# Kernel optimization log

Hardware: AMD Instinct MI355X
Metric: run time of the kernel (lower is better)

The kernel has to match this reference:

```python
import jax, jax.numpy as jnp
import numpy as np

N, D_IN, D_OUT, E = 100000, 64, 64, 800000
C_IN, C_OUT = 1.0, 1.0
MAX_NORM = 1e6   # manifold.max_norm clamp used by PseudoHypAgg
EPS = 1e-15
BALL_EPS = 4e-3  # Poincare-ball projection margin (fp32)


def _artanh(x):
    return jnp.arctanh(jnp.clip(x, -1 + 1e-7, 1 - 1e-7))


def _proj(x, c):
    # project onto the open Poincare ball of curvature c
    sqrt_c = jnp.sqrt(c)
    norm = jnp.clip(jnp.linalg.norm(x, axis=-1, keepdims=True), EPS)
    maxn = (1.0 - BALL_EPS) / sqrt_c
    return jnp.where(norm > maxn, x / norm * maxn, x)


def _expmap0(u, c):
    sqrt_c = jnp.sqrt(c)
    n = jnp.clip(jnp.linalg.norm(u, axis=-1, keepdims=True), EPS)
    return jnp.tanh(sqrt_c * n) * u / (sqrt_c * n)


def _logmap0(p, c):
    sqrt_c = jnp.sqrt(c)
    n = jnp.clip(jnp.linalg.norm(p, axis=-1, keepdims=True), EPS)
    return _artanh(sqrt_c * n) * p / (sqrt_c * n)


def _mobius_add(x, y, c):
    x2 = jnp.sum(x * x, -1, keepdims=True)
    y2 = jnp.sum(y * y, -1, keepdims=True)
    xy = jnp.sum(x * y, -1, keepdims=True)
    num = (1 + 2 * c * xy + c * y2) * x + (1 - c * x2) * y
    den = 1 + 2 * c * xy + c * c * x2 * y2
    return num / jnp.clip(den, EPS)


def _mobius_matvec(M, x, c):
    sqrt_c = jnp.sqrt(c)
    x_norm = jnp.clip(jnp.linalg.norm(x, axis=-1, keepdims=True), EPS)
    mx = x @ M.T  # [N, D_OUT]
    mx_norm = jnp.clip(jnp.linalg.norm(mx, axis=-1, keepdims=True), EPS)
    res = jnp.tanh(mx_norm / x_norm * _artanh(sqrt_c * x_norm)) * mx / (mx_norm * sqrt_c)
    zero = jnp.all(mx == 0, axis=-1, keepdims=True)
    return jnp.where(zero, jnp.zeros_like(res), res)


def setup_inputs() -> dict:
    key = jax.random.key(0)
    k1, k2, k3, k4, k5, k6 = jax.random.split(key, 6)
    # node features: small-norm points inside the unit ball
    x = _proj(0.05 * jax.random.normal(k1, (N, D_IN), jnp.float32), C_IN)
    W = jax.random.normal(k2, (D_OUT, D_IN), jnp.float32) / np.float32(np.sqrt(D_IN))
    b = 0.01 * jax.random.normal(k3, (D_OUT,), jnp.float32)
    edge_row = jax.random.randint(k4, (E,), 0, N, jnp.int32)
    edge_col = jax.random.randint(k5, (E,), 0, N, jnp.int32)
    edge_val = jax.random.uniform(k6, (E,), jnp.float32) / 16.0  # ~normalized adj weights
    return {"x": x, "W": W, "b": b, "edge_row": edge_row,
            "edge_col": edge_col, "edge_val": edge_val}


def reference(x, W, b, edge_row, edge_col, edge_val):
    # --- PseudoHypLinear (eval mode: dropout inactive) ---
    mv = _mobius_matvec(W, x, C_IN)
    res = _proj(mv, C_IN)
    hyp_b = _proj(_expmap0(b[None, :], C_IN), C_IN)  # proj_tan0 is identity on the ball
    h = _proj(_mobius_add(res, hyp_b, C_IN), C_IN)
    # --- PseudoHypAgg (use_att=False): spmm in tangent space at origin ---
    x_t = _logmap0(h, C_IN)                              # [N, D_OUT]
    msg = edge_val[:, None] * x_t[edge_col]              # [E, D_OUT]
    support_t = jax.ops.segment_sum(msg, edge_row, num_segments=N)
    support_t = jnp.minimum(support_t, MAX_NORM)         # clamp(max=manifold.max_norm)
    h = _proj(_expmap0(support_t, C_IN), C_IN)           # proj_tan0 identity
    # --- PseudoHypAct: act in tangent at origin (c_in), re-embed with c_out ---
    xt = jax.nn.relu(_logmap0(h, C_IN))
    return _proj(_expmap0(xt, C_OUT), C_OUT)
```

## Files before the change

kernel.cpp:

```cpp
#include <hip/hip_runtime.h>
#include <hip/hip_fp16.h>
#include <math.h>

#define DD 64
#define BK 128
#define BCAP 2048
#define NBKT_MAX 800
#define CHUNK 8192
constexpr float FEPS = 1e-15f;
constexpr float MAXN = 1.0f - 4e-3f;

__device__ __forceinline__ float wsum(float v) {
    v += __shfl_xor(v, 32);
    v += __shfl_xor(v, 16);
    v += __shfl_xor(v, 8);
    v += __shfl_xor(v, 4);
    v += __shfl_xor(v, 2);
    v += __shfl_xor(v, 1);
    return v;
}

__device__ __forceinline__ int wave_incl_scan(int v) {
    int lane = threadIdx.x & 63;
    #pragma unroll
    for (int d = 1; d < 64; d <<= 1) {
        int t = __shfl_up(v, d);
        if (lane >= d) v += t;
    }
    return v;
}

__device__ __forceinline__ float artanh_c(float x) {
    x = fminf(fmaxf(x, -1.f + 1e-7f), 1.f - 1e-7f);
    return 0.5f * logf((1.f + x) / (1.f - x));
}

__global__ void khb_kernel(const float* __restrict__ b, float* __restrict__ hbuf) {
    int lane = threadIdx.x;
    float bv = b[lane];
    float n2 = wsum(bv * bv);
    float n = fmaxf(sqrtf(n2), FEPS);
    float th = tanhf(n);
    float p = th * (bv / n);
    float pn = th * (sqrtf(n2) / n);
    float pn_c = fmaxf(pn, FEPS);
    if (pn_c > MAXN) p *= MAXN / pn_c;
    float p2 = wsum(p * p);
    hbuf[lane] = p;
    if (lane == 0) hbuf[DD] = p2;
}

__global__ __launch_bounds__(512) void klinear(
    const float* __restrict__ x, const float* __restrict__ W,
    const float* __restrict__ hbuf, __half* __restrict__ xth, int n_nodes) {
    __shared__ float tile[DD * 65];
    __shared__ float red0[8][DD];
    __shared__ float red1[8][DD];
    const int t = threadIdx.x;
    const int lane = t & 63;
    const int w = t >> 6;
    const int n0 = blockIdx.x * DD;

    #pragma unroll
    for (int rep = 0; rep < 2; ++rep) {
        int i = rep * 512 + t;
        int nd = i >> 4, q = i & 15;
        int node = n0 + nd;
        const float4* src = reinterpret_cast<const float4*>(
            x + (size_t)(node < n_nodes ? node : 0) * DD);
        float4 v = src[q];
        float* d = &tile[nd * 65 + q * 4];
        d[0] = v.x; d[1] = v.y; d[2] = v.z; d[3] = v.w;
    }
    __syncthreads();

    const int jbase = __builtin_amdgcn_readfirstlane(w) * 8;
    float mx[8] = {0.f, 0.f, 0.f, 0.f, 0.f, 0.f, 0.f, 0.f};
    float xn2 = 0.f;
    #pragma unroll
    for (int kk = 0; kk < 4; ++kk) {
        float xv[16];
        #pragma unroll
        for (int ki = 0; ki < 16; ++ki)
            xv[ki] = tile[lane * 65 + kk * 16 + ki];
        #pragma unroll
        for (int ki = 0; ki < 16; ++ki)
            xn2 = fmaf(xv[ki], xv[ki], xn2);
        #pragma unroll
        for (int jj = 0; jj < 8; ++jj) {
            const float* Wr = W + (jbase + jj) * DD + kk * 16;
            float a = mx[jj];
            #pragma unroll
            for (int ki = 0; ki < 16; ++ki) a = fmaf(Wr[ki], xv[ki], a);
            mx[jj] = a;
        }
    }
    float mx2p = 0.f, mxhp = 0.f;
    #pragma unroll
    for (int jj = 0; jj < 8; ++jj) {
        mx2p = fmaf(mx[jj], mx[jj], mx2p);
        mxhp = fmaf(mx[jj], hbuf[jbase + jj], mxhp);
    }
    red0[w][lane] = mx2p;
    red1[w][lane] = mxhp;
    __syncthreads();
    float mx2 = 0.f, mxh = 0.f;
    #pragma unroll
    for (int ww = 0; ww < 8; ++ww) {
        mx2 += red0[ww][lane];
        mxh += red1[ww][lane];
    }

    float xn = fmaxf(sqrtf(xn2), FEPS);
    float mxn = fmaxf(sqrtf(mx2), FEPS);
    float th = tanhf((mxn / xn) * artanh_c(xn));
    float sres = (mx2 == 0.f) ? 0.f : th / mxn;
    float rn = (mx2 == 0.f) ? 0.f : th * (sqrtf(mx2) / mxn);
    float rn_c = fmaxf(rn, FEPS);
    float s1 = (rn_c > MAXN) ? sres * (MAXN / rn_c) : sres;
    float x2r = s1 * s1 * mx2;
    float xy = s1 * mxh;
    float y2 = hbuf[DD];
    float ca = 1.f + 2.f * xy + y2;
    float cb = 1.f - x2r;
    float rden = 1.f / fmaxf(1.f + 2.f * xy + x2r * y2, FEPS);
    float al = ca * s1 * rden;
    float be = cb * rden;
    float h2 = al * al * mx2 + 2.f * al * be * mxh + be * be * y2;
    float hn = fmaxf(sqrtf(h2), FEPS);
    float sh = 1.f;
    if (hn > MAXN) { sh = MAXN / hn; hn = MAXN; }
    float su = sh * (artanh_c(hn) / hn);
    float A = su * al, B = su * be;

    #pragma unroll
    for (int jj = 0; jj < 8; ++jj)
        tile[lane * 65 + jbase + jj] = fmaf(A, mx[jj], B * hbuf[jbase + jj]);
    __syncthreads();

    uint2* dst = reinterpret_cast<uint2*>(xth + (size_t)n0 * DD);
    #pragma unroll
    for (int rep = 0; rep < 2; ++rep) {
        int i = rep * 512 + t;
        int nd = i >> 4, q = i & 15;
        if (n0 + nd < n_nodes) {
            const float* s = &tile[nd * 65 + q * 4];
            __half2 h0 = __floats2half2_rn(s[0], s[1]);
            __half2 h1 = __floats2half2_rn(s[2], s[3]);
            uint2 o;
            o.x = *reinterpret_cast<unsigned int*>(&h0);
            o.y = *reinterpret_cast<unsigned int*>(&h1);
            dst[i] = o;
        }
    }
}

__global__ __launch_bounds__(512) void kbin(
    const int* __restrict__ erow, const int* __restrict__ ecol,
    const float* __restrict__ eval_, int* __restrict__ gcnt,
    int2* __restrict__ binned, int nbkt, int n_edges) {
    __shared__ int lcnt[NBKT_MAX];
    __shared__ int goff[NBKT_MAX];
    const int t = threadIdx.x;
    const int eb = blockIdx.x * CHUNK;
    for (int i = t; i < nbkt; i += 512) lcnt[i] = 0;
    __syncthreads();
    int rk[16];
    int rowv[16];
    #pragma unroll
    for (int i = 0; i < 16; ++i) {
        int e = eb + i * 512 + t;
        rk[i] = -1;
        if (e < n_edges) {
            int r = erow[e];
            rowv[i] = r;
            int bkt = r >> 7;
            int rank = atomicAdd(&lcnt[bkt], 1);
            rk[i] = (bkt << 13) | rank;
        }
    }
    __syncthreads();
    for (int i = t; i < nbkt; i += 512) {
        int c = lcnt[i];
        if (c > 0) goff[i] = atomicAdd(&gcnt[i], c);
    }
    __syncthreads();
    #pragma unroll
    for (int i = 0; i < 16; ++i) {
        int e = eb + i * 512 + t;
        if (e >= n_edges) continue;
        int bkt = rk[i] >> 13, rank = rk[i] & 8191;
        int pos = goff[bkt] + rank;
        if (pos < BCAP) {
            int lr = rowv[i] & (BK - 1);
            binned[(size_t)bkt * BCAP + pos] =
                make_int2((lr << 17) | ecol[e], __float_as_int(eval_[e]));
        }
    }
}

__device__ __forceinline__ void agg_epilogue(
    float4 acc, int row, int fl, float* __restrict__ out) {
    float4 s;
    s.x = fminf(acc.x, 1e6f); s.y = fminf(acc.y, 1e6f);
    s.z = fminf(acc.z, 1e6f); s.w = fminf(acc.w, 1e6f);
    float4 rs;
    rs.x = fmaxf(s.x, 0.f); rs.y = fmaxf(s.y, 0.f);
    rs.z = fmaxf(s.z, 0.f); rs.w = fmaxf(s.w, 0.f);
    float n2p = s.x * s.x + s.y * s.y + s.z * s.z + s.w * s.w;
    float sp2p = rs.x * rs.x + rs.y * rs.y + rs.z * rs.z + rs.w * rs.w;
    #pragma unroll
    for (int m = 1; m < 16; m <<= 1) {
        n2p += __shfl_xor(n2p, m);
        sp2p += __shfl_xor(sp2p, m);
    }
    float n = fmaxf(sqrtf(n2p), FEPS);
    float th = tanhf(n);
    float c1 = th / n;
    float pn = th * (sqrtf(n2p) / n);
    float pn_c = fmaxf(pn, FEPS);
    if (pn_c > MAXN) { c1 *= MAXN / pn_c; pn_c = MAXN; }
    float k1 = (artanh_c(pn_c) / pn_c) * c1;
    float u2 = k1 * k1 * sp2p;
    float un = fmaxf(sqrtf(u2), FEPS);
    float t2 = tanhf(un);
    float k2 = (t2 / un) * k1;
    float on = t2 * (sqrtf(u2) / un);
    float on_c = fmaxf(on, FEPS);
    if (on_c > MAXN) k2 *= MAXN / on_c;
    float4 o;
    o.x = k2 * rs.x; o.y = k2 * rs.y; o.z = k2 * rs.z; o.w = k2 * rs.w;
    reinterpret_cast<float4*>(out)[(size_t)row * 16 + fl] = o;
}

__global__ __launch_bounds__(256) void kagg2(
    const int* __restrict__ gcnt, const int2* __restrict__ binned,
    const __half* __restrict__ xth, float* __restrict__ out, int n_nodes) {
    __shared__ int hist[BK], offs[BK], cur[BK];
    __shared__ int2 srt[BCAP];
    const int t = threadIdx.x;
    const int b = blockIdx.x;
    for (int i = t; i < BK; i += 256) hist[i] = 0;
    __syncthreads();
    const int nrec = min(gcnt[b], BCAP);
    const int2* rec = binned + (size_t)b * BCAP;
    int2 rc[BCAP / 256];
    #pragma unroll
    for (int i = 0; i < BCAP / 256; ++i) {
        int j = i * 256 + t;
        if (j < nrec) {
            rc[i] = rec[j];
            atomicAdd(&hist[rc[i].x >> 17], 1);
        }
    }
    __syncthreads();
    if (t < 64) {
        int v = hist[t];
        int s = wave_incl_scan(v);
        offs[t] = s - v;
    }
    __syncthreads();
    if (t < 64) {
        int c = offs[63] + hist[63];
        int v = hist[64 + t];
        int s = wave_incl_scan(v);
        offs[64 + t] = c + s - v;
    }
    __syncthreads();
    for (int i = t; i < BK; i += 256) cur[i] = offs[i];
    __syncthreads();
    #pragma unroll
    for (int i = 0; i < BCAP / 256; ++i) {
        int j = i * 256 + t;
        if (j < nrec) {
            int lr = rc[i].x >> 17;
            int p = atomicAdd(&cur[lr], 1);
            srt[p] = make_int2(rc[i].x & 0x1FFFF, rc[i].y);
        }
    }
    __syncthreads();

    const int g = t >> 4, fl = t & 15;
    #pragma unroll
    for (int it = 0; it < BK / 16; ++it) {
        int lr = it * 16 + g;
        int row = b * BK + lr;
        if (row >= n_nodes) continue;
        int beg = offs[lr], end = beg + hist[lr];
        float4 acc = make_float4(0.f, 0.f, 0.f, 0.f);
        int j = beg;
        for (; j + 1 < end; j += 2) {
            int2 e0 = srt[j], e1 = srt[j + 1];
            float2 r0 = *reinterpret_cast<const float2*>(
                xth + (size_t)e0.x * DD + fl * 4);
            float2 r1 = *reinterpret_cast<const float2*>(
                xth + (size_t)e1.x * DD + fl * 4);
            float w0 = __int_as_float(e0.y), w1 = __int_as_float(e1.y);
            float2 a0 = __half22float2(*reinterpret_cast<__half2*>(&r0.x));
            float2 a1 = __half22float2(*reinterpret_cast<__half2*>(&r0.y));
            float2 b0 = __half22float2(*reinterpret_cast<__half2*>(&r1.x));
            float2 b1 = __half22float2(*reinterpret_cast<__half2*>(&r1.y));
            acc.x = fmaf(w0, a0.x, acc.x); acc.y = fmaf(w0, a0.y, acc.y);
            acc.z = fmaf(w0, a1.x, acc.z); acc.w = fmaf(w0, a1.y, acc.w);
            acc.x = fmaf(w1, b0.x, acc.x); acc.y = fmaf(w1, b0.y, acc.y);
            acc.z = fmaf(w1, b1.x, acc.z); acc.w = fmaf(w1, b1.y, acc.w);
        }
        if (j < end) {
            int2 e = srt[j];
            float2 r0 = *reinterpret_cast<const float2*>(
                xth + (size_t)e.x * DD + fl * 4);
            float w0 = __int_as_float(e.y);
            float2 a0 = __half22float2(*reinterpret_cast<__half2*>(&r0.x));
            float2 a1 = __half22float2(*reinterpret_cast<__half2*>(&r0.y));
            acc.x = fmaf(w0, a0.x, acc.x); acc.y = fmaf(w0, a0.y, acc.y);
            acc.z = fmaf(w0, a1.x, acc.z); acc.w = fmaf(w0, a1.y, acc.w);
        }
        agg_epilogue(acc, row, fl, out);
    }
}

extern "C" void kernel_launch(void* const* d_in, const int* in_sizes, int n_in,
                              void* d_out, int out_size, void* d_ws, size_t ws_size,
                              hipStream_t stream) {
    const float* x     = (const float*)d_in[0];
    const float* W     = (const float*)d_in[1];
    const float* b     = (const float*)d_in[2];
    const int*   erow  = (const int*)d_in[3];
    const int*   ecol  = (const int*)d_in[4];
    const float* eval_ = (const float*)d_in[5];
    const int n_nodes = in_sizes[0] / DD;
    const int n_edges = in_sizes[3];
    float* out = (float*)d_out;

    const int NBKT = (n_nodes + BK - 1) / BK;

    int2*   binned = (int2*)d_ws;
    __half* xth    = (__half*)(binned + (size_t)NBKT * BCAP);
    float*  hbuf   = (float*)(xth + (size_t)n_nodes * DD);
    int*    gcnt   = (int*)(hbuf + 80);

    const int nbB = (n_edges + CHUNK - 1) / CHUNK;
    const int nbL = (n_nodes + DD - 1) / DD;

    hipMemsetAsync(gcnt, 0, NBKT_MAX * sizeof(int), stream);
    khb_kernel<<<1, 64, 0, stream>>>(b, hbuf);
    kbin<<<nbB, 512, 0, stream>>>(erow, ecol, eval_, gcnt, binned, NBKT, n_edges);
    klinear<<<nbL, 512, 0, stream>>>(x, W, hbuf, xth, n_nodes);
    kagg2<<<NBKT, 256, 0, stream>>>(gcnt, binned, xth, out, n_nodes);
}
```

Baseline: 161.4 us.

## Fuse bias, binning and linear kernels into one launch; widen aggregation blocks

```diff
diff --git a/kernel.cpp b/kernel.cpp
--- a/kernel.cpp
+++ b/kernel.cpp
@@ -35,28 +35,61 @@
     return 0.5f * logf((1.f + x) / (1.f - x));
 }
 
-__global__ void khb_kernel(const float* __restrict__ b, float* __restrict__ hbuf) {
-    int lane = threadIdx.x;
-    float bv = b[lane];
-    float n2 = wsum(bv * bv);
-    float n = fmaxf(sqrtf(n2), FEPS);
-    float th = tanhf(n);
-    float p = th * (bv / n);
-    float pn = th * (sqrtf(n2) / n);
-    float pn_c = fmaxf(pn, FEPS);
-    if (pn_c > MAXN) p *= MAXN / pn_c;
-    float p2 = wsum(p * p);
-    hbuf[lane] = p;
-    if (lane == 0) hbuf[DD] = p2;
-}
-
-__global__ __launch_bounds__(512) void klinear(
+struct SmemLin {
+    float tile[DD * 65];
+    float red0[8][DD];
+    float red1[8][DD];
+    float hb[66];
+};
+struct SmemBin {
+    int lcnt[NBKT_MAX];
+    int goff[NBKT_MAX];
+};
+
+__global__ __launch_bounds__(512) void kfused(
     const float* __restrict__ x, const float* __restrict__ W,
-    const float* __restrict__ hbuf, __half* __restrict__ xth, int n_nodes) {
-    __shared__ float tile[DD * 65];
-    __shared__ float red0[8][DD];
-    __shared__ float red1[8][DD];
+    const float* __restrict__ bvec, __half* __restrict__ xth,
+    const int* __restrict__ erow, const int* __restrict__ ecol,
+    const float* __restrict__ eval_, int* __restrict__ gcnt,
+    int2* __restrict__ binned, int nbkt, int n_edges, int n_nodes, int nbL) {
+    __shared__ union { SmemLin lin; SmemBin bin; } sm;
     const int t = threadIdx.x;
+
+    if ((int)blockIdx.x >= nbL) {
+        const int eb = ((int)blockIdx.x - nbL) * CHUNK;
+        for (int i = t; i < nbkt; i += 512) sm.bin.lcnt[i] = 0;
+        __syncthreads();
+        int rk[16];
+        #pragma unroll
+        for (int i = 0; i < 16; ++i) {
+            int e = eb + i * 512 + t;
+            rk[i] = -1;
+            if (e < n_edges) {
+                int r = erow[e];
+                int bkt = r >> 7;
+                int rank = atomicAdd(&sm.bin.lcnt[bkt], 1);
+                rk[i] = (bkt << 20) | ((r & (BK - 1)) << 13) | rank;
+            }
+        }
+        __syncthreads();
+        for (int i = t; i < nbkt; i += 512) {
+            int c = sm.bin.lcnt[i];
+            if (c > 0) sm.bin.goff[i] = atomicAdd(&gcnt[i], c);
+        }
+        __syncthreads();
+        #pragma unroll
+        for (int i = 0; i < 16; ++i) {
+            int e = eb + i * 512 + t;
+            if (e >= n_edges) continue;
+            int bkt = rk[i] >> 20, lr = (rk[i] >> 13) & 127, rank = rk[i] & 8191;
+            int pos = sm.bin.goff[bkt] + rank;
+            if (pos < BCAP)
+                binned[(size_t)bkt * BCAP + pos] =
+                    make_int2((lr << 17) | ecol[e], __float_as_int(eval_[e]));
+        }
+        return;
+    }
+
     const int lane = t & 63;
     const int w = t >> 6;
     const int n0 = blockIdx.x * DD;
@@ -69,8 +102,21 @@
         const float4* src = reinterpret_cast<const float4*>(
             x + (size_t)(node < n_nodes ? node : 0) * DD);
         float4 v = src[q];
-        float* d = &tile[nd * 65 + q * 4];
+        float* d = &sm.lin.tile[nd * 65 + q * 4];
         d[0] = v.x; d[1] = v.y; d[2] = v.z; d[3] = v.w;
+    }
+    if (t < 64) {
+        float bv = bvec[t];
+        float n2 = wsum(bv * bv);
+        float n = fmaxf(sqrtf(n2), FEPS);
+        float th = tanhf(n);
+        float p = th * (bv / n);
+        float pn = th * (sqrtf(n2) / n);
+        float pn_c = fmaxf(pn, FEPS);
+        if (pn_c > MAXN) p *= MAXN / pn_c;
+        sm.lin.hb[t] = p;
+        float p2 = wsum(p * p);
+        if (t == 0) sm.lin.hb[DD] = p2;
     }
     __syncthreads();
 
@@ -82,7 +128,7 @@
         float xv[16];
         #pragma unroll
         for (int ki = 0; ki < 16; ++ki)
-            xv[ki] = tile[lane * 65 + kk * 16 + ki];
+            xv[ki] = sm.lin.tile[lane * 65 + kk * 16 + ki];
         #pragma unroll
         for (int ki = 0; ki < 16; ++ki)
             xn2 = fmaf(xv[ki], xv[ki], xn2);
@@ -99,16 +145,16 @@
     #pragma unroll
     for (int jj = 0; jj < 8; ++jj) {
         mx2p = fmaf(mx[jj], mx[jj], mx2p);
-        mxhp = fmaf(mx[jj], hbuf[jbase + jj], mxhp);
-    }
-    red0[w][lane] = mx2p;
-    red1[w][lane] = mxhp;
+        mxhp = fmaf(mx[jj], sm.lin.hb[jbase + jj], mxhp);
+    }
+    sm.lin.red0[w][lane] = mx2p;
+    sm.lin.red1[w][lane] = mxhp;
     __syncthreads();
     float mx2 = 0.f, mxh = 0.f;
     #pragma unroll
     for (int ww = 0; ww < 8; ++ww) {
-        mx2 += red0[ww][lane];
-        mxh += red1[ww][lane];
+        mx2 += sm.lin.red0[ww][lane];
+        mxh += sm.lin.red1[ww][lane];
     }
 
     float xn = fmaxf(sqrtf(xn2), FEPS);
@@ -120,7 +166,7 @@
     float s1 = (rn_c > MAXN) ? sres * (MAXN / rn_c) : sres;
     float x2r = s1 * s1 * mx2;
     float xy = s1 * mxh;
-    float y2 = hbuf[DD];
+    float y2 = sm.lin.hb[DD];
     float ca = 1.f + 2.f * xy + y2;
     float cb = 1.f - x2r;
     float rden = 1.f / fmaxf(1.f + 2.f * xy + x2r * y2, FEPS);
@@ -135,7 +181,8 @@
 
     #pragma unroll
     for (int jj = 0; jj < 8; ++jj)
-        tile[lane * 65 + jbase + jj] = fmaf(A, mx[jj], B * hbuf[jbase + jj]);
+        sm.lin.tile[lane * 65 + jbase + jj] =
+            fmaf(A, mx[jj], B * sm.lin.hb[jbase + jj]);
     __syncthreads();
 
     uint2* dst = reinterpret_cast<uint2*>(xth + (size_t)n0 * DD);
@@ -144,57 +191,13 @@
         int i = rep * 512 + t;
         int nd = i >> 4, q = i & 15;
         if (n0 + nd < n_nodes) {
-            const float* s = &tile[nd * 65 + q * 4];
+            const float* s = &sm.lin.tile[nd * 65 + q * 4];
             __half2 h0 = __floats2half2_rn(s[0], s[1]);
             __half2 h1 = __floats2half2_rn(s[2], s[3]);
             uint2 o;
             o.x = *reinterpret_cast<unsigned int*>(&h0);
             o.y = *reinterpret_cast<unsigned int*>(&h1);
             dst[i] = o;
-        }
-    }
-}
-
-__global__ __launch_bounds__(512) void kbin(
-    const int* __restrict__ erow, const int* __restrict__ ecol,
-    const float* __restrict__ eval_, int* __restrict__ gcnt,
-    int2* __restrict__ binned, int nbkt, int n_edges) {
-    __shared__ int lcnt[NBKT_MAX];
-    __shared__ int goff[NBKT_MAX];
-    const int t = threadIdx.x;
-    const int eb = blockIdx.x * CHUNK;
-    for (int i = t; i < nbkt; i += 512) lcnt[i] = 0;
-    __syncthreads();
-    int rk[16];
-    int rowv[16];
-    #pragma unroll
-    for (int i = 0; i < 16; ++i) {
-        int e = eb + i * 512 + t;
-        rk[i] = -1;
-        if (e < n_edges) {
-            int r = erow[e];
-            rowv[i] = r;
-            int bkt = r >> 7;
-            int rank = atomicAdd(&lcnt[bkt], 1);
-            rk[i] = (bkt << 13) | rank;
-        }
-    }
-    __syncthreads();
-    for (int i = t; i < nbkt; i += 512) {
-        int c = lcnt[i];
-        if (c > 0) goff[i] = atomicAdd(&gcnt[i], c);
-    }
-    __syncthreads();
-    #pragma unroll
-    for (int i = 0; i < 16; ++i) {
-        int e = eb + i * 512 + t;
-        if (e >= n_edges) continue;
-        int bkt = rk[i] >> 13, rank = rk[i] & 8191;
-        int pos = goff[bkt] + rank;
-        if (pos < BCAP) {
-            int lr = rowv[i] & (BK - 1);
-            binned[(size_t)bkt * BCAP + pos] =
-                make_int2((lr << 17) | ecol[e], __float_as_int(eval_[e]));
         }
     }
 }
@@ -233,21 +236,21 @@
     reinterpret_cast<float4*>(out)[(size_t)row * 16 + fl] = o;
 }
 
-__global__ __launch_bounds__(256) void kagg2(
+__global__ __launch_bounds__(512) void kagg2(
     const int* __restrict__ gcnt, const int2* __restrict__ binned,
     const __half* __restrict__ xth, float* __restrict__ out, int n_nodes) {
     __shared__ int hist[BK], offs[BK], cur[BK];
     __shared__ int2 srt[BCAP];
     const int t = threadIdx.x;
     const int b = blockIdx.x;
-    for (int i = t; i < BK; i += 256) hist[i] = 0;
+    for (int i = t; i < BK; i += 512) hist[i] = 0;
     __syncthreads();
     const int nrec = min(gcnt[b], BCAP);
     const int2* rec = binned + (size_t)b * BCAP;
-    int2 rc[BCAP / 256];
-    #pragma unroll
-    for (int i = 0; i < BCAP / 256; ++i) {
-        int j = i * 256 + t;
+    int2 rc[BCAP / 512];
+    #pragma unroll
+    for (int i = 0; i < BCAP / 512; ++i) {
+        int j = i * 512 + t;
         if (j < nrec) {
             rc[i] = rec[j];
             atomicAdd(&hist[rc[i].x >> 17], 1);
@@ -267,11 +270,11 @@
         offs[64 + t] = c + s - v;
     }
     __syncthreads();
-    for (int i = t; i < BK; i += 256) cur[i] = offs[i];
-    __syncthreads();
-    #pragma unroll
-    for (int i = 0; i < BCAP / 256; ++i) {
-        int j = i * 256 + t;
+    for (int i = t; i < BK; i += 512) cur[i] = offs[i];
+    __syncthreads();
+    #pragma unroll
+    for (int i = 0; i < BCAP / 512; ++i) {
+        int j = i * 512 + t;
         if (j < nrec) {
             int lr = rc[i].x >> 17;
             int p = atomicAdd(&cur[lr], 1);
@@ -282,33 +285,41 @@
 
     const int g = t >> 4, fl = t & 15;
     #pragma unroll
-    for (int it = 0; it < BK / 16; ++it) {
-        int lr = it * 16 + g;
+    for (int it = 0; it < BK / 32; ++it) {
+        int lr = it * 32 + g;
         int row = b * BK + lr;
         if (row >= n_nodes) continue;
         int beg = offs[lr], end = beg + hist[lr];
         float4 acc = make_float4(0.f, 0.f, 0.f, 0.f);
         int j = beg;
-        for (; j + 1 < end; j += 2) {
-            int2 e0 = srt[j], e1 = srt[j + 1];
-            float2 r0 = *reinterpret_cast<const float2*>(
-                xth + (size_t)e0.x * DD + fl * 4);
-            float2 r1 = *reinterpret_cast<const float2*>(
-                xth + (size_t)e1.x * DD + fl * 4);
+        for (; j + 3 < end; j += 4) {
+            int2 e0 = srt[j], e1 = srt[j + 1], e2 = srt[j + 2], e3 = srt[j + 3];
+            float2 r0 = *reinterpret_cast<const float2*>(xth + (size_t)e0.x * DD + fl * 4);
+            float2 r1 = *reinterpret_cast<const float2*>(xth + (size_t)e1.x * DD + fl * 4);
+            float2 r2 = *reinterpret_cast<const float2*>(xth + (size_t)e2.x * DD + fl * 4);
+            float2 r3 = *reinterpret_cast<const float2*>(xth + (size_t)e3.x * DD + fl * 4);
             float w0 = __int_as_float(e0.y), w1 = __int_as_float(e1.y);
+            float w2 = __int_as_float(e2.y), w3 = __int_as_float(e3.y);
             float2 a0 = __half22float2(*reinterpret_cast<__half2*>(&r0.x));
             float2 a1 = __half22float2(*reinterpret_cast<__half2*>(&r0.y));
             float2 b0 = __half22float2(*reinterpret_cast<__half2*>(&r1.x));
             float2 b1 = __half22float2(*reinterpret_cast<__half2*>(&r1.y));
+            float2 c0 = __half22float2(*reinterpret_cast<__half2*>(&r2.x));
+            float2 c1 = __half22float2(*reinterpret_cast<__half2*>(&r2.y));
+            float2 d0 = __half22float2(*reinterpret_cast<__half2*>(&r3.x));
+            float2 d1 = __half22float2(*reinterpret_cast<__half2*>(&r3.y));
             acc.x = fmaf(w0, a0.x, acc.x); acc.y = fmaf(w0, a0.y, acc.y);
             acc.z = fmaf(w0, a1.x, acc.z); acc.w = fmaf(w0, a1.y, acc.w);
             acc.x = fmaf(w1, b0.x, acc.x); acc.y = fmaf(w1, b0.y, acc.y);
             acc.z = fmaf(w1, b1.x, acc.z); acc.w = fmaf(w1, b1.y, acc.w);
-        }
-        if (j < end) {
+            acc.x = fmaf(w2, c0.x, acc.x); acc.y = fmaf(w2, c0.y, acc.y);
+            acc.z = fmaf(w2, c1.x, acc.z); acc.w = fmaf(w2, c1.y, acc.w);
+            acc.x = fmaf(w3, d0.x, acc.x); acc.y = fmaf(w3, d0.y, acc.y);
+            acc.z = fmaf(w3, d1.x, acc.z); acc.w = fmaf(w3, d1.y, acc.w);
+        }
+        for (; j < end; ++j) {
             int2 e = srt[j];
-            float2 r0 = *reinterpret_cast<const float2*>(
-                xth + (size_t)e.x * DD + fl * 4);
+            float2 r0 = *reinterpret_cast<const float2*>(xth + (size_t)e.x * DD + fl * 4);
             float w0 = __int_as_float(e.y);
             float2 a0 = __half22float2(*reinterpret_cast<__half2*>(&r0.x));
             float2 a1 = __half22float2(*reinterpret_cast<__half2*>(&r0.y));
@@ -336,15 +347,13 @@
 
     int2*   binned = (int2*)d_ws;
     __half* xth    = (__half*)(binned + (size_t)NBKT * BCAP);
-    float*  hbuf   = (float*)(xth + (size_t)n_nodes * DD);
-    int*    gcnt   = (int*)(hbuf + 80);
+    int*    gcnt   = (int*)(xth + (size_t)n_nodes * DD);
 
     const int nbB = (n_edges + CHUNK - 1) / CHUNK;
     const int nbL = (n_nodes + DD - 1) / DD;
 
     hipMemsetAsync(gcnt, 0, NBKT_MAX * sizeof(int), stream);
-    khb_kernel<<<1, 64, 0, stream>>>(b, hbuf);
-    kbin<<<nbB, 512, 0, stream>>>(erow, ecol, eval_, gcnt, binned, NBKT, n_edges);
-    klinear<<<nbL, 512, 0, stream>>>(x, W, hbuf, xth, n_nodes);
-    kagg2<<<NBKT, 256, 0, stream>>>(gcnt, binned, xth, out, n_nodes);
-}
+    kfused<<<nbL + nbB, 512, 0, stream>>>(x, W, b, xth, erow, ecol, eval_,
+                                          gcnt, binned, NBKT, n_edges, n_nodes, nbL);
+    kagg2<<<NBKT, 512, 0, stream>>>(gcnt, binned, xth, out, n_nodes);
+}
```

Result: faster. 148.8 us (-7.8%).
